# Kernel tuning notes

Hardware: AMD Instinct MI355X
Metric: run time of the kernel (lower is better)

## Reference

```python
import jax, jax.numpy as jnp
import numpy as np

D_PAIR = 128
NUM_HEADS = 4
LN_EPS = 1e-5


def _mha(x, w_in, b_in, w_out, b_out, num_heads):
    # x: [B, R, S, D]; attention over axis S (keys) for each query position.
    B, R, S, D = x.shape
    hd = D // num_heads
    qkv = jnp.einsum('brsd,ed->brse', x, w_in) + b_in  # [B,R,S,3D]
    q, k, v = jnp.split(qkv, 3, axis=-1)
    q = q.reshape(B, R, S, num_heads, hd)
    k = k.reshape(B, R, S, num_heads, hd)
    v = v.reshape(B, R, S, num_heads, hd)
    scores = jnp.einsum('brqhd,brkhd->brhqk', q, k) / jnp.sqrt(jnp.asarray(hd, x.dtype))
    attn = jax.nn.softmax(scores, axis=-1)
    out = jnp.einsum('brhqk,brkhd->brqhd', attn, v).reshape(B, R, S, D)
    return jnp.einsum('brsd,ed->brse', out, w_out) + b_out


def _layernorm(x, gamma, beta):
    mu = jnp.mean(x, axis=-1, keepdims=True)
    var = jnp.mean(jnp.square(x - mu), axis=-1, keepdims=True)
    return (x - mu) * jax.lax.rsqrt(var + LN_EPS) * gamma + beta


def setup_inputs() -> dict:
    key = jax.random.key(0)
    ks = jax.random.split(key, 12)
    B, L, D = 1, 256, D_PAIR
    s = 0.02
    return {
        'pair_repr': jax.random.normal(ks[0], (B, L, L, D), dtype=jnp.float32),
        'chain_id_tensor': jax.random.randint(ks[1], (L,), 0, 2),
        'w_in_s': jax.random.normal(ks[2], (3 * D, D), dtype=jnp.float32) * s,
        'b_in_s': jnp.zeros((3 * D,), jnp.float32),
        'w_out_s': jax.random.normal(ks[3], (D, D), dtype=jnp.float32) * s,
        'b_out_s': jnp.zeros((D,), jnp.float32),
        'w_in_e': jax.random.normal(ks[4], (3 * D, D), dtype=jnp.float32) * s,
        'b_in_e': jnp.zeros((3 * D,), jnp.float32),
        'w_out_e': jax.random.normal(ks[5], (D, D), dtype=jnp.float32) * s,
        'b_out_e': jnp.zeros((D,), jnp.float32),
        'gamma_s': jnp.ones((D,), jnp.float32),
        'beta_s': jnp.zeros((D,), jnp.float32),
        'gamma_e': jnp.ones((D,), jnp.float32),
        'beta_e': jnp.zeros((D,), jnp.float32),
        'w_gate': jax.random.normal(ks[6], (D, D), dtype=jnp.float32) * s,
        'b_gate': jnp.zeros((D,), jnp.float32),
    }


def reference(pair_repr, chain_id_tensor, w_in_s, b_in_s, w_out_s, b_out_s,
              w_in_e, b_in_e, w_out_e, b_out_e, gamma_s, beta_s,
              gamma_e, beta_e, w_gate, b_gate):
    # Row-wise (starting node) attention: attend over axis 2.
    attn_i = _mha(pair_repr, w_in_s, b_in_s, w_out_s, b_out_s, NUM_HEADS)
    pair = _layernorm(pair_repr + attn_i, gamma_s, beta_s)
    # Column-wise (ending node) attention: transpose rows/cols, attend, transpose back.
    pair_t = jnp.swapaxes(pair, 1, 2)
    attn_j = _mha(pair_t, w_in_e, b_in_e, w_out_e, b_out_e, NUM_HEADS)
    pair = _layernorm(pair + jnp.swapaxes(attn_j, 1, 2), gamma_e, beta_e)
    gate = jax.nn.sigmoid(jnp.einsum('bijd,ed->bije', pair, w_gate) + b_gate)
    return pair * gate
```

## Files before the change

### kernel.cpp

```cpp
#include <hip/hip_runtime.h>
#include <hip/hip_bf16.h>
#include <cstddef>

#define DD 128

typedef unsigned short u16;
typedef short short8v __attribute__((ext_vector_type(8)));
typedef float floatx4 __attribute__((ext_vector_type(4)));

__device__ __forceinline__ u16 f2b(float x) {
    unsigned u = __float_as_uint(x);
    return (u16)((u + 0x7FFF + ((u >> 16) & 1)) >> 16);
}
__device__ __forceinline__ unsigned cvtpk_bf16(float lo, float hi) {
    unsigned r;
    asm("v_cvt_pk_bf16_f32 %0, %1, %2" : "=v"(r) : "v"(lo), "v"(hi));
    return r;
}

__global__ __launch_bounds__(512) void wcvt_kernel(
    const float* __restrict__ a0, const float* __restrict__ a1,
    const float* __restrict__ a2, const float* __restrict__ a3,
    const float* __restrict__ a4, u16* __restrict__ dst)
{
    int q = blockIdx.x * 512 + threadIdx.x;
    int i = q * 4;
    const float* src; int off;
    if      (i < 49152)  { src = a0; off = 0; }
    else if (i < 65536)  { src = a1; off = 49152; }
    else if (i < 114688) { src = a2; off = 65536; }
    else if (i < 131072) { src = a3; off = 114688; }
    else                 { src = a4; off = 131072; }
    float4 v = *reinterpret_cast<const float4*>(src + (i - off));
    ushort4 o = { f2b(v.x), f2b(v.y), f2b(v.z), f2b(v.w) };
    *reinterpret_cast<ushort4*>(dst + i) = o;
}

__device__ __forceinline__ void stage_wb(const u16* __restrict__ Wb,
                                         u16* __restrict__ Wl, int tid) {
    #pragma unroll
    for (int it = 0; it < 4; ++it) {
        int f = tid + it * 512;
        int row = f >> 4, c8 = f & 15;
        uint4 v = *reinterpret_cast<const uint4*>(Wb + (size_t)row * DD + c8 * 8);
        *reinterpret_cast<uint4*>(&Wl[row * 136 + c8 * 8]) = v;
    }
}

__global__ __launch_bounds__(512) void proj_qkv_mfma(
    const float* __restrict__ Xf, const u16* __restrict__ Xb,
    const u16* __restrict__ Wb, const float* __restrict__ bias,
    __hip_bfloat16* __restrict__ QKo, __hip_bfloat16* __restrict__ VTo)
{
    __shared__ u16 Wl[128 * 136];
    const int tid = threadIdx.x;
    const int tok0 = blockIdx.x * 128;
    const int lane = tid & 63, wq = tid >> 6;
    const int lq = lane & 15, g = lane >> 4;
    const int t = tok0 + wq * 16 + lq;

    short8v bfrag[4];
    if (Xb) {
        #pragma unroll
        for (int ks = 0; ks < 4; ++ks)
            bfrag[ks] = *reinterpret_cast<const short8v*>(Xb + (size_t)t * DD + ks * 32 + g * 8);
    } else {
        #pragma unroll
        for (int ks = 0; ks < 4; ++ks) {
            const float* p = Xf + (size_t)t * DD + ks * 32 + g * 8;
            float4 a = *reinterpret_cast<const float4*>(p);
            float4 b = *reinterpret_cast<const float4*>(p + 4);
            u16 tmp[8] = { f2b(a.x), f2b(a.y), f2b(a.z), f2b(a.w),
                           f2b(b.x), f2b(b.y), f2b(b.z), f2b(b.w) };
            bfrag[ks] = *reinterpret_cast<const short8v*>(tmp);
        }
    }

    u16* qkt = reinterpret_cast<u16*>(QKo) + (size_t)t * 256;
    u16* vtb = reinterpret_cast<u16*>(VTo);
    const int rr_ = t >> 8, kk_ = t & 255;

    for (int c = 0; c < 3; ++c) {
        if (c) __syncthreads();
        stage_wb(Wb + (size_t)c * 128 * DD, Wl, tid);
        __syncthreads();
        #pragma unroll
        for (int et = 0; et < 8; ++et) {
            float4 b4 = *reinterpret_cast<const float4*>(bias + c * 128 + et * 16 + g * 4);
            floatx4 acc = { b4.x, b4.y, b4.z, b4.w };
            #pragma unroll
            for (int ks = 0; ks < 4; ++ks) {
                short8v afrag = *reinterpret_cast<const short8v*>(
                    &Wl[(et * 16 + lq) * 136 + ks * 32 + g * 8]);
                acc = __builtin_amdgcn_mfma_f32_16x16x32_bf16(afrag, bfrag[ks], acc, 0, 0, 0);
            }
            if (c < 2) {
                ushort4 o;
                o.x = f2b(acc[0]); o.y = f2b(acc[1]); o.z = f2b(acc[2]); o.w = f2b(acc[3]);
                *reinterpret_cast<ushort4*>(&qkt[c * 128 + et * 16 + g * 4]) = o;
            } else {
                int e = et * 16 + g * 4;
                int hh = e >> 5, dbase = e & 31;
                u16* vb = vtb + ((size_t)(rr_ * 4 + hh) * 32 + dbase) * 256 + kk_;
                vb[0]   = f2b(acc[0]);
                vb[256] = f2b(acc[1]);
                vb[512] = f2b(acc[2]);
                vb[768] = f2b(acc[3]);
            }
        }
    }
}

__global__ __launch_bounds__(512, 6) void attn_mfma_kernel(
    const __hip_bfloat16* __restrict__ QK, const __hip_bfloat16* __restrict__ VT,
    __hip_bfloat16* __restrict__ O, int swap_store)
{
    constexpr int KP = 40;
    constexpr int VP = 264;
    __shared__ u16 K_lds[256 * KP];
    __shared__ u16 Vt_lds[32 * VP];

    const int tid = threadIdx.x;
    const int h = blockIdx.x, r = blockIdx.y;
    const u16* qk = reinterpret_cast<const u16*>(QK) + (size_t)r * 256 * 256;
    const u16* vt = reinterpret_cast<const u16*>(VT) + ((size_t)r * 4 + h) * 8192;

    #pragma unroll
    for (int it = 0; it < 2; ++it) {
        int f = tid + it * 512;
        int row = f >> 2, c = f & 3;
        uint4 v = *reinterpret_cast<const uint4*>(qk + (size_t)row * 256 + 128 + h * 32 + c * 8);
        *reinterpret_cast<uint4*>(&K_lds[row * KP + c * 8]) = v;
    }
    #pragma unroll
    for (int it = 0; it < 2; ++it) {
        int f = tid + it * 512;
        int row = f >> 5, c = f & 31;
        uint4 v = *reinterpret_cast<const uint4*>(vt + row * 256 + c * 8);
        *reinterpret_cast<uint4*>(&Vt_lds[row * VP + c * 8]) = v;
    }
    __syncthreads();

    const int lane = tid & 63;
    const int wq = tid >> 6;
    const int lq = lane & 15;
    const int g  = lane >> 4;
    const int bp0 = ((g & 1) * 32 + lq) * 4;
    const int bp1 = bp0 + 64;
    const bool hi_half = lane >= 32;
    const float C1 = 0.25505654196988f;

    #pragma unroll
    for (int mq = 0; mq < 2; ++mq) {
        const int q0 = wq * 32 + mq * 16;
        short8v qfrag = *reinterpret_cast<const short8v*>(
            qk + (size_t)(q0 + lq) * 256 + h * 32 + g * 8);

        floatx4 s[16];
        __builtin_amdgcn_s_setprio(1);
        #pragma unroll
        for (int ni = 0; ni < 16; ++ni) {
            short8v kfrag = *reinterpret_cast<const short8v*>(&K_lds[(ni * 16 + lq) * KP + g * 8]);
            floatx4 z = {0.f, 0.f, 0.f, 0.f};
            s[ni] = __builtin_amdgcn_mfma_f32_16x16x32_bf16(kfrag, qfrag, z, 0, 0, 0);
        }
        __builtin_amdgcn_s_setprio(0);

        float m = -1e30f;
        #pragma unroll
        for (int ni = 0; ni < 16; ++ni)
            m = fmaxf(fmaxf(fmaxf(m, s[ni][0]), fmaxf(s[ni][1], s[ni][2])), s[ni][3]);
        m = fmaxf(m, __shfl_xor(m, 16));
        m = fmaxf(m, __shfl_xor(m, 32));
        const float m1 = m * C1;

        float ell = 0.f;
        unsigned u[32];
        #pragma unroll
        for (int ni = 0; ni < 16; ++ni) {
            float p0 = __builtin_amdgcn_exp2f(__builtin_fmaf(s[ni][0], C1, -m1));
            float p1 = __builtin_amdgcn_exp2f(__builtin_fmaf(s[ni][1], C1, -m1));
            float p2 = __builtin_amdgcn_exp2f(__builtin_fmaf(s[ni][2], C1, -m1));
            float p3 = __builtin_amdgcn_exp2f(__builtin_fmaf(s[ni][3], C1, -m1));
            ell += (p0 + p1) + (p2 + p3);
            u[2 * ni]     = cvtpk_bf16(p0, p1);
            u[2 * ni + 1] = cvtpk_bf16(p2, p3);
        }
        ell += __shfl_xor(ell, 16);
        ell += __shfl_xor(ell, 32);

        floatx4 o0 = {0.f, 0.f, 0.f, 0.f}, o1 = {0.f, 0.f, 0.f, 0.f};
        __builtin_amdgcn_s_setprio(1);
        #pragma unroll
        for (int ks = 0; ks < 8; ++ks) {
            unsigned Y0 = hi_half ? u[4 * ks + 2] : u[4 * ks];
            unsigned Y1 = hi_half ? u[4 * ks + 3] : u[4 * ks + 1];
            int w0 = __builtin_amdgcn_ds_bpermute(bp0, (int)Y0);
            int w1 = __builtin_amdgcn_ds_bpermute(bp0, (int)Y1);
            int w2 = __builtin_amdgcn_ds_bpermute(bp1, (int)Y0);
            int w3 = __builtin_amdgcn_ds_bpermute(bp1, (int)Y1);
            union { int i[4]; short8v v; } pu;
            pu.i[0] = w0; pu.i[1] = w1; pu.i[2] = w2; pu.i[3] = w3;
            short8v v0 = *reinterpret_cast<const short8v*>(&Vt_lds[lq * VP + ks * 32 + g * 8]);
            short8v v1 = *reinterpret_cast<const short8v*>(&Vt_lds[(16 + lq) * VP + ks * 32 + g * 8]);
            o0 = __builtin_amdgcn_mfma_f32_16x16x32_bf16(v0, pu.v, o0, 0, 0, 0);
            o1 = __builtin_amdgcn_mfma_f32_16x16x32_bf16(v1, pu.v, o1, 0, 0, 0);
        }
        __builtin_amdgcn_s_setprio(0);

        const float inv = 1.f / ell;
        const size_t opos = swap_store ? ((size_t)(q0 + lq) * 256 + r)
                                       : ((size_t)r * 256 + q0 + lq);
        __hip_bfloat16* orow = O + opos * 128 + h * 32;
        ushort4 w0s, w1s;
        w0s.x = f2b(o0[0] * inv); w0s.y = f2b(o0[1] * inv);
        w0s.z = f2b(o0[2] * inv); w0s.w = f2b(o0[3] * inv);
        w1s.x = f2b(o1[0] * inv); w1s.y = f2b(o1[1] * inv);
        w1s.z = f2b(o1[2] * inv); w1s.w = f2b(o1[3] * inv);
        *reinterpret_cast<ushort4*>(reinterpret_cast<u16*>(orow) + g * 4) = w0s;
        *reinterpret_cast<ushort4*>(reinterpret_cast<u16*>(orow) + 16 + g * 4) = w1s;
    }
}

__global__ __launch_bounds__(512) void proj_ln_mfma(
    const __hip_bfloat16* __restrict__ A, const u16* __restrict__ Wb,
    const float* __restrict__ bias, const float* __restrict__ RES,
    const float* __restrict__ gamma, const float* __restrict__ beta,
    float* __restrict__ OUT, u16* __restrict__ Xt)
{
    __shared__ u16 Wl[128 * 136];
    const int tid = threadIdx.x;
    const int tok0 = blockIdx.x * 128;
    const int lane = tid & 63, wq = tid >> 6;
    const int lq = lane & 15, g = lane >> 4;
    const int t = tok0 + wq * 16 + lq;
    const u16* A16 = reinterpret_cast<const u16*>(A);

    stage_wb(Wb, Wl, tid);

    short8v bfrag[4];
    #pragma unroll
    for (int ks = 0; ks < 4; ++ks)
        bfrag[ks] = *reinterpret_cast<const short8v*>(A16 + (size_t)t * DD + ks * 32 + g * 8);

    __syncthreads();

    floatx4 acc[8];
    #pragma unroll
    for (int et = 0; et < 8; ++et) {
        float4 b4 = *reinterpret_cast<const float4*>(bias + et * 16 + g * 4);
        float4 r4 = *reinterpret_cast<const float4*>(RES + (size_t)t * DD + et * 16 + g * 4);
        acc[et] = { b4.x + r4.x, b4.y + r4.y, b4.z + r4.z, b4.w + r4.w };
        #pragma unroll
        for (int ks = 0; ks < 4; ++ks) {
            short8v afrag = *reinterpret_cast<const short8v*>(
                &Wl[(et * 16 + lq) * 136 + ks * 32 + g * 8]);
            acc[et] = __builtin_amdgcn_mfma_f32_16x16x32_bf16(afrag, bfrag[ks], acc[et], 0, 0, 0);
        }
    }

    float s = 0.f, ss = 0.f;
    #pragma unroll
    for (int et = 0; et < 8; ++et)
        #pragma unroll
        for (int rr = 0; rr < 4; ++rr) { float v = acc[et][rr]; s += v; ss += v * v; }
    s  += __shfl_xor(s, 16);  s  += __shfl_xor(s, 32);
    ss += __shfl_xor(ss, 16); ss += __shfl_xor(ss, 32);
    float mu = s * (1.f / 128.f);
    float var = ss * (1.f / 128.f) - mu * mu;
    float rstd = rsqrtf(var + 1e-5f);

    u16* xt = Xt + (size_t)((t & 255) * 256 + (t >> 8)) * DD;
    #pragma unroll
    for (int et = 0; et < 8; ++et) {
        float4 g4 = *reinterpret_cast<const float4*>(gamma + et * 16 + g * 4);
        float4 be4 = *reinterpret_cast<const float4*>(beta + et * 16 + g * 4);
        float4 o4;
        o4.x = (acc[et][0] - mu) * rstd * g4.x + be4.x;
        o4.y = (acc[et][1] - mu) * rstd * g4.y + be4.y;
        o4.z = (acc[et][2] - mu) * rstd * g4.z + be4.z;
        o4.w = (acc[et][3] - mu) * rstd * g4.w + be4.w;
        *reinterpret_cast<float4*>(OUT + (size_t)t * DD + et * 16 + g * 4) = o4;
        ushort4 xb = { f2b(o4.x), f2b(o4.y), f2b(o4.z), f2b(o4.w) };
        *reinterpret_cast<ushort4*>(&xt[et * 16 + g * 4]) = xb;
    }
}

__global__ __launch_bounds__(512) void proj_ln_gate_mfma(
    const __hip_bfloat16* __restrict__ A, const u16* __restrict__ Wb,
    const float* __restrict__ bias, const float* __restrict__ RES,
    const float* __restrict__ gamma, const float* __restrict__ beta,
    const u16* __restrict__ Wgb, const float* __restrict__ bg,
    float* __restrict__ OUT)
{
    __shared__ u16 Wl[128 * 136];
    __shared__ u16 Yl[128 * 136];
    const int tid = threadIdx.x;
    const int tok0 = blockIdx.x * 128;
    const int lane = tid & 63, wq = tid >> 6;
    const int lq = lane & 15, g = lane >> 4;
    const int tl = wq * 16 + lq;
    const int t = tok0 + tl;
    const u16* A16 = reinterpret_cast<const u16*>(A);

    stage_wb(Wb, Wl, tid);

    short8v bfrag[4];
    #pragma unroll
    for (int ks = 0; ks < 4; ++ks)
        bfrag[ks] = *reinterpret_cast<const short8v*>(A16 + (size_t)t * DD + ks * 32 + g * 8);

    __syncthreads();

    floatx4 acc[8];
    #pragma unroll
    for (int et = 0; et < 8; ++et) {
        float4 b4 = *reinterpret_cast<const float4*>(bias + et * 16 + g * 4);
        float4 r4 = *reinterpret_cast<const float4*>(RES + (size_t)t * DD + et * 16 + g * 4);
        acc[et] = { b4.x + r4.x, b4.y + r4.y, b4.z + r4.z, b4.w + r4.w };
        #pragma unroll
        for (int ks = 0; ks < 4; ++ks) {
            short8v afrag = *reinterpret_cast<const short8v*>(
                &Wl[(et * 16 + lq) * 136 + ks * 32 + g * 8]);
            acc[et] = __builtin_amdgcn_mfma_f32_16x16x32_bf16(afrag, bfrag[ks], acc[et], 0, 0, 0);
        }
    }

    float s = 0.f, ss = 0.f;
    #pragma unroll
    for (int et = 0; et < 8; ++et)
        #pragma unroll
        for (int rr = 0; rr < 4; ++rr) { float v = acc[et][rr]; s += v; ss += v * v; }
    s  += __shfl_xor(s, 16);  s  += __shfl_xor(s, 32);
    ss += __shfl_xor(ss, 16); ss += __shfl_xor(ss, 32);
    float mu = s * (1.f / 128.f);
    float var = ss * (1.f / 128.f) - mu * mu;
    float rstd = rsqrtf(var + 1e-5f);

    #pragma unroll
    for (int et = 0; et < 8; ++et) {
        float4 g4 = *reinterpret_cast<const float4*>(gamma + et * 16 + g * 4);
        float4 be4 = *reinterpret_cast<const float4*>(beta + et * 16 + g * 4);
        acc[et][0] = (acc[et][0] - mu) * rstd * g4.x + be4.x;
        acc[et][1] = (acc[et][1] - mu) * rstd * g4.y + be4.y;
        acc[et][2] = (acc[et][2] - mu) * rstd * g4.z + be4.z;
        acc[et][3] = (acc[et][3] - mu) * rstd * g4.w + be4.w;
        ushort4 yb;
        yb.x = f2b(acc[et][0]); yb.y = f2b(acc[et][1]);
        yb.z = f2b(acc[et][2]); yb.w = f2b(acc[et][3]);
        *reinterpret_cast<ushort4*>(&Yl[tl * 136 + et * 16 + g * 4]) = yb;
    }

    __syncthreads();
    stage_wb(Wgb, Wl, tid);
    __syncthreads();

    short8v yfrag[4];
    #pragma unroll
    for (int ks = 0; ks < 4; ++ks)
        yfrag[ks] = *reinterpret_cast<const short8v*>(&Yl[tl * 136 + ks * 32 + g * 8]);

    #pragma unroll
    for (int et = 0; et < 8; ++et) {
        float4 b4 = *reinterpret_cast<const float4*>(bg + et * 16 + g * 4);
        floatx4 z = { b4.x, b4.y, b4.z, b4.w };
        #pragma unroll
        for (int ks = 0; ks < 4; ++ks) {
            short8v afrag = *reinterpret_cast<const short8v*>(
                &Wl[(et * 16 + lq) * 136 + ks * 32 + g * 8]);
            z = __builtin_amdgcn_mfma_f32_16x16x32_bf16(afrag, yfrag[ks], z, 0, 0, 0);
        }
        float4 o4;
        o4.x = acc[et][0] / (1.f + __expf(-z[0]));
        o4.y = acc[et][1] / (1.f + __expf(-z[1]));
        o4.z = acc[et][2] / (1.f + __expf(-z[2]));
        o4.w = acc[et][3] / (1.f + __expf(-z[3]));
        *reinterpret_cast<float4*>(OUT + (size_t)t * DD + et * 16 + g * 4) = o4;
    }
}

extern "C" void kernel_launch(void* const* d_in, const int* in_sizes, int n_in,
                              void* d_out, int out_size, void* d_ws, size_t ws_size,
                              hipStream_t stream) {
    const float* pair    = (const float*)d_in[0];
    const float* w_in_s  = (const float*)d_in[2];
    const float* b_in_s  = (const float*)d_in[3];
    const float* w_out_s = (const float*)d_in[4];
    const float* b_out_s = (const float*)d_in[5];
    const float* w_in_e  = (const float*)d_in[6];
    const float* b_in_e  = (const float*)d_in[7];
    const float* w_out_e = (const float*)d_in[8];
    const float* b_out_e = (const float*)d_in[9];
    const float* gamma_s = (const float*)d_in[10];
    const float* beta_s  = (const float*)d_in[11];
    const float* gamma_e = (const float*)d_in[12];
    const float* beta_e  = (const float*)d_in[13];
    const float* w_gate  = (const float*)d_in[14];
    const float* b_gate  = (const float*)d_in[15];
    float* out = (float*)d_out;

    __hip_bfloat16* qk   = (__hip_bfloat16*)d_ws;
    __hip_bfloat16* vt   = qk + (size_t)65536 * 256;
    __hip_bfloat16* attn = vt + (size_t)1024 * 32 * 256;
    u16*            xt   = (u16*)(attn + (size_t)65536 * 128);
    u16*            wb   = xt + (size_t)65536 * 128;

    wcvt_kernel<<<80, 512, 0, stream>>>(w_in_s, w_out_s, w_in_e, w_out_e, w_gate, wb);

    proj_qkv_mfma<<<512, 512, 0, stream>>>(pair, nullptr, wb, b_in_s, qk, vt);
    attn_mfma_kernel<<<dim3(4, 256), 512, 0, stream>>>(qk, vt, attn, 0);
    proj_ln_mfma<<<512, 512, 0, stream>>>(attn, wb + 49152, b_out_s, pair,
                                          gamma_s, beta_s, out, xt);
    proj_qkv_mfma<<<512, 512, 0, stream>>>(nullptr, xt, wb + 65536, b_in_e, qk, vt);
    attn_mfma_kernel<<<dim3(4, 256), 512, 0, stream>>>(qk, vt, attn, 1);
    proj_ln_gate_mfma<<<512, 512, 0, stream>>>(attn, wb + 114688, b_out_e, out,
                                               gamma_e, beta_e, wb + 131072, b_gate,
                                               out);
}
```

Before: 142.7 us.

## Switch attention to 32x32x16 MFMA with permlane swaps and head-major output layout

Rewrites the attention kernel so each wave computes a 32-query tile with 32x32x16 bf16 MFMAs instead of two 16-query passes with 16x16x32 MFMAs. The P-matrix relayout now uses v_permlane32_swap instead of ds_bpermute, and the row reductions use a single permlane swap. The attention output is stored head-major ([h][token][32]) and the projection kernels read their B fragments from that layout. The larger accumulators raise register pressure, so the launch-bounds occupancy hint drops from 6 to 3.

```diff
diff --git a/kernel.cpp b/kernel.cpp
--- a/kernel.cpp
+++ b/kernel.cpp
@@ -7,6 +7,7 @@
 typedef unsigned short u16;
 typedef short short8v __attribute__((ext_vector_type(8)));
 typedef float floatx4 __attribute__((ext_vector_type(4)));
+typedef float floatx16 __attribute__((ext_vector_type(16)));
 
 __device__ __forceinline__ u16 f2b(float x) {
     unsigned u = __float_as_uint(x);
@@ -111,7 +112,7 @@
     }
 }
 
-__global__ __launch_bounds__(512, 6) void attn_mfma_kernel(
+__global__ __launch_bounds__(512, 3) void attn_mfma_kernel(
     const __hip_bfloat16* __restrict__ QK, const __hip_bfloat16* __restrict__ VT,
     __hip_bfloat16* __restrict__ O, int swap_store)
 {
@@ -122,7 +123,7 @@
 
     const int tid = threadIdx.x;
     const int h = blockIdx.x, r = blockIdx.y;
-    const u16* qk = reinterpret_cast<const u16*>(QK) + (size_t)r * 256 * 256;
+    const u16* qk = reinterpret_cast<const u16*>(QK) + (size_t)r * 65536;
     const u16* vt = reinterpret_cast<const u16*>(VT) + ((size_t)r * 4 + h) * 8192;
 
     #pragma unroll
@@ -143,82 +144,90 @@
 
     const int lane = tid & 63;
     const int wq = tid >> 6;
-    const int lq = lane & 15;
-    const int g  = lane >> 4;
-    const int bp0 = ((g & 1) * 32 + lq) * 4;
-    const int bp1 = bp0 + 64;
-    const bool hi_half = lane >= 32;
+    const int ql = lane & 31;
+    const int hi = lane >> 5;
+    const int q0 = wq * 32;
     const float C1 = 0.25505654196988f;
 
-    #pragma unroll
-    for (int mq = 0; mq < 2; ++mq) {
-        const int q0 = wq * 32 + mq * 16;
-        short8v qfrag = *reinterpret_cast<const short8v*>(
-            qk + (size_t)(q0 + lq) * 256 + h * 32 + g * 8);
-
-        floatx4 s[16];
-        __builtin_amdgcn_s_setprio(1);
-        #pragma unroll
-        for (int ni = 0; ni < 16; ++ni) {
-            short8v kfrag = *reinterpret_cast<const short8v*>(&K_lds[(ni * 16 + lq) * KP + g * 8]);
-            floatx4 z = {0.f, 0.f, 0.f, 0.f};
-            s[ni] = __builtin_amdgcn_mfma_f32_16x16x32_bf16(kfrag, qfrag, z, 0, 0, 0);
-        }
-        __builtin_amdgcn_s_setprio(0);
-
-        float m = -1e30f;
-        #pragma unroll
-        for (int ni = 0; ni < 16; ++ni)
-            m = fmaxf(fmaxf(fmaxf(m, s[ni][0]), fmaxf(s[ni][1], s[ni][2])), s[ni][3]);
-        m = fmaxf(m, __shfl_xor(m, 16));
-        m = fmaxf(m, __shfl_xor(m, 32));
-        const float m1 = m * C1;
-
-        float ell = 0.f;
-        unsigned u[32];
-        #pragma unroll
-        for (int ni = 0; ni < 16; ++ni) {
-            float p0 = __builtin_amdgcn_exp2f(__builtin_fmaf(s[ni][0], C1, -m1));
-            float p1 = __builtin_amdgcn_exp2f(__builtin_fmaf(s[ni][1], C1, -m1));
-            float p2 = __builtin_amdgcn_exp2f(__builtin_fmaf(s[ni][2], C1, -m1));
-            float p3 = __builtin_amdgcn_exp2f(__builtin_fmaf(s[ni][3], C1, -m1));
+    short8v qf0 = *reinterpret_cast<const short8v*>(
+        qk + (size_t)(q0 + ql) * 256 + h * 32 + hi * 8);
+    short8v qf1 = *reinterpret_cast<const short8v*>(
+        qk + (size_t)(q0 + ql) * 256 + h * 32 + 16 + hi * 8);
+
+    const floatx16 zf = {0.f,0.f,0.f,0.f,0.f,0.f,0.f,0.f,
+                         0.f,0.f,0.f,0.f,0.f,0.f,0.f,0.f};
+
+    floatx16 sacc[8];
+    #pragma unroll
+    for (int b = 0; b < 8; ++b) sacc[b] = zf;
+    __builtin_amdgcn_s_setprio(1);
+    #pragma unroll
+    for (int b = 0; b < 8; ++b) {
+        short8v k0 = *reinterpret_cast<const short8v*>(&K_lds[(32 * b + ql) * KP + hi * 8]);
+        short8v k1 = *reinterpret_cast<const short8v*>(&K_lds[(32 * b + ql) * KP + 16 + hi * 8]);
+        sacc[b] = __builtin_amdgcn_mfma_f32_32x32x16_bf16(k0, qf0, sacc[b], 0, 0, 0);
+        sacc[b] = __builtin_amdgcn_mfma_f32_32x32x16_bf16(k1, qf1, sacc[b], 0, 0, 0);
+    }
+    __builtin_amdgcn_s_setprio(0);
+
+    float m = -1e30f;
+    #pragma unroll
+    for (int b = 0; b < 8; ++b)
+        #pragma unroll
+        for (int rr = 0; rr < 16; ++rr) m = fmaxf(m, sacc[b][rr]);
+    {
+        float mx = m, my = m;
+        asm("v_permlane32_swap_b32 %0, %1" : "+v"(mx), "+v"(my));
+        m = fmaxf(mx, my);
+    }
+    const float m1 = m * C1;
+
+    float ell = 0.f;
+    unsigned u[64];
+    #pragma unroll
+    for (int b = 0; b < 8; ++b) {
+        #pragma unroll
+        for (int e = 0; e < 4; ++e) {
+            float p0 = __builtin_amdgcn_exp2f(__builtin_fmaf(sacc[b][4*e+0], C1, -m1));
+            float p1 = __builtin_amdgcn_exp2f(__builtin_fmaf(sacc[b][4*e+1], C1, -m1));
+            float p2 = __builtin_amdgcn_exp2f(__builtin_fmaf(sacc[b][4*e+2], C1, -m1));
+            float p3 = __builtin_amdgcn_exp2f(__builtin_fmaf(sacc[b][4*e+3], C1, -m1));
             ell += (p0 + p1) + (p2 + p3);
-            u[2 * ni]     = cvtpk_bf16(p0, p1);
-            u[2 * ni + 1] = cvtpk_bf16(p2, p3);
-        }
-        ell += __shfl_xor(ell, 16);
-        ell += __shfl_xor(ell, 32);
-
-        floatx4 o0 = {0.f, 0.f, 0.f, 0.f}, o1 = {0.f, 0.f, 0.f, 0.f};
-        __builtin_amdgcn_s_setprio(1);
-        #pragma unroll
-        for (int ks = 0; ks < 8; ++ks) {
-            unsigned Y0 = hi_half ? u[4 * ks + 2] : u[4 * ks];
-            unsigned Y1 = hi_half ? u[4 * ks + 3] : u[4 * ks + 1];
-            int w0 = __builtin_amdgcn_ds_bpermute(bp0, (int)Y0);
-            int w1 = __builtin_amdgcn_ds_bpermute(bp0, (int)Y1);
-            int w2 = __builtin_amdgcn_ds_bpermute(bp1, (int)Y0);
-            int w3 = __builtin_amdgcn_ds_bpermute(bp1, (int)Y1);
-            union { int i[4]; short8v v; } pu;
-            pu.i[0] = w0; pu.i[1] = w1; pu.i[2] = w2; pu.i[3] = w3;
-            short8v v0 = *reinterpret_cast<const short8v*>(&Vt_lds[lq * VP + ks * 32 + g * 8]);
-            short8v v1 = *reinterpret_cast<const short8v*>(&Vt_lds[(16 + lq) * VP + ks * 32 + g * 8]);
-            o0 = __builtin_amdgcn_mfma_f32_16x16x32_bf16(v0, pu.v, o0, 0, 0, 0);
-            o1 = __builtin_amdgcn_mfma_f32_16x16x32_bf16(v1, pu.v, o1, 0, 0, 0);
-        }
-        __builtin_amdgcn_s_setprio(0);
-
-        const float inv = 1.f / ell;
-        const size_t opos = swap_store ? ((size_t)(q0 + lq) * 256 + r)
-                                       : ((size_t)r * 256 + q0 + lq);
-        __hip_bfloat16* orow = O + opos * 128 + h * 32;
-        ushort4 w0s, w1s;
-        w0s.x = f2b(o0[0] * inv); w0s.y = f2b(o0[1] * inv);
-        w0s.z = f2b(o0[2] * inv); w0s.w = f2b(o0[3] * inv);
-        w1s.x = f2b(o1[0] * inv); w1s.y = f2b(o1[1] * inv);
-        w1s.z = f2b(o1[2] * inv); w1s.w = f2b(o1[3] * inv);
-        *reinterpret_cast<ushort4*>(reinterpret_cast<u16*>(orow) + g * 4) = w0s;
-        *reinterpret_cast<ushort4*>(reinterpret_cast<u16*>(orow) + 16 + g * 4) = w1s;
+            u[8*b + 2*e]     = cvtpk_bf16(p0, p1);
+            u[8*b + 2*e + 1] = cvtpk_bf16(p2, p3);
+        }
+    }
+    {
+        float ex = ell, ey = ell;
+        asm("v_permlane32_swap_b32 %0, %1" : "+v"(ex), "+v"(ey));
+        ell = ex + ey;
+    }
+
+    floatx16 acc = zf;
+    __builtin_amdgcn_s_setprio(1);
+    #pragma unroll
+    for (int kb = 0; kb < 16; ++kb) {
+        const int b = kb >> 1, be = kb & 1;
+        int a0 = (int)u[8*b + 4*be + 2], b0 = (int)u[8*b + 4*be + 0];
+        asm("v_permlane32_swap_b32 %0, %1" : "+v"(a0), "+v"(b0));
+        int a1 = (int)u[8*b + 4*be + 3], b1 = (int)u[8*b + 4*be + 1];
+        asm("v_permlane32_swap_b32 %0, %1" : "+v"(a1), "+v"(b1));
+        union { int i[4]; short8v v; } pu;
+        pu.i[0] = b0; pu.i[1] = b1; pu.i[2] = a0; pu.i[3] = a1;
+        short8v vf = *reinterpret_cast<const short8v*>(&Vt_lds[ql * VP + kb * 16 + hi * 8]);
+        acc = __builtin_amdgcn_mfma_f32_32x32x16_bf16(vf, pu.v, acc, 0, 0, 0);
+    }
+    __builtin_amdgcn_s_setprio(0);
+
+    const float inv = 1.f / ell;
+    const int q = q0 + ql;
+    const size_t opos = swap_store ? ((size_t)q * 256 + r) : ((size_t)r * 256 + q);
+    u16* ob = reinterpret_cast<u16*>(O) + (size_t)h * 2097152 + opos * 32;
+    #pragma unroll
+    for (int e = 0; e < 4; ++e) {
+        ushort4 w = { f2b(acc[4*e+0] * inv), f2b(acc[4*e+1] * inv),
+                      f2b(acc[4*e+2] * inv), f2b(acc[4*e+3] * inv) };
+        *reinterpret_cast<ushort4*>(ob + e * 8 + hi * 4) = w;
     }
 }
 
@@ -241,7 +250,8 @@
     short8v bfrag[4];
     #pragma unroll
     for (int ks = 0; ks < 4; ++ks)
-        bfrag[ks] = *reinterpret_cast<const short8v*>(A16 + (size_t)t * DD + ks * 32 + g * 8);
+        bfrag[ks] = *reinterpret_cast<const short8v*>(
+            A16 + (size_t)ks * 2097152 + (size_t)t * 32 + g * 8);
 
     __syncthreads();
 
@@ -308,7 +318,8 @@
     short8v bfrag[4];
     #pragma unroll
     for (int ks = 0; ks < 4; ++ks)
-        bfrag[ks] = *reinterpret_cast<const short8v*>(A16 + (size_t)t * DD + ks * 32 + g * 8);
+        bfrag[ks] = *reinterpret_cast<const short8v*>(
+            A16 + (size_t)ks * 2097152 + (size_t)t * 32 + g * 8);
 
     __syncthreads();
 
```

Measured after the change: 140.6 us. About the same (-1.5%).
